# Kernel tuning notes

Measured on AMD Instinct MI355X. Metric: run time of the kernel, lower is better.

The kernel has to match this reference:

```python
import jax, jax.numpy as jnp
import numpy as np

D_MODEL = 1024
N_HEADS = 16
HEAD_DIM = D_MODEL // N_HEADS
D_FF = 4096
RANK = 8
B, T = 4, 2048


def _layernorm(x, g, b, eps=1e-5):
    mu = jnp.mean(x, axis=-1, keepdims=True)
    var = jnp.var(x, axis=-1, keepdims=True)
    return (x - mu) * jax.lax.rsqrt(var + eps) * g + b


def _dyn_linear(x, W, A, b_dyn, bias=None):
    # base: x [b,t,i] @ W.T  (W is [o,i] like nn.Linear)
    out = jnp.einsum('bti,oi->bto', x, W)
    if bias is not None:
        out = out + bias
    # per-sample low-rank delta: (x @ b_dyn.T) @ A.T
    delta = jnp.einsum('bti,bri,or->bto', x, b_dyn, A)
    return out + delta


def setup_inputs() -> dict:
    key = jax.random.key(0)
    ks = jax.random.split(key, 24)
    s = 0.02
    inp = {
        'x': jax.random.normal(ks[0], (B, T, D_MODEL), jnp.float32),
        'dyn_q': jax.random.normal(ks[1], (B, RANK, D_MODEL), jnp.float32) * s,
        'dyn_k': jax.random.normal(ks[2], (B, RANK, D_MODEL), jnp.float32) * s,
        'dyn_v': jax.random.normal(ks[3], (B, RANK, D_MODEL), jnp.float32) * s,
        'dyn_ff1': jax.random.normal(ks[4], (B, RANK, D_MODEL), jnp.float32) * s,
        'dyn_ff2': jax.random.normal(ks[5], (B, RANK, D_FF), jnp.float32) * s,
        'Wq': jax.random.normal(ks[6], (D_MODEL, D_MODEL), jnp.float32) / np.sqrt(D_MODEL),
        'Aq': jax.random.normal(ks[7], (D_MODEL, RANK), jnp.float32) * s,
        'Wk': jax.random.normal(ks[8], (D_MODEL, D_MODEL), jnp.float32) / np.sqrt(D_MODEL),
        'Ak': jax.random.normal(ks[9], (D_MODEL, RANK), jnp.float32) * s,
        'Wv': jax.random.normal(ks[10], (D_MODEL, D_MODEL), jnp.float32) / np.sqrt(D_MODEL),
        'Av': jax.random.normal(ks[11], (D_MODEL, RANK), jnp.float32) * s,
        'Wo': jax.random.normal(ks[12], (D_MODEL, D_MODEL), jnp.float32) / np.sqrt(D_MODEL),
        'W1': jax.random.normal(ks[13], (D_FF, D_MODEL), jnp.float32) / np.sqrt(D_MODEL),
        'b1': jnp.zeros((D_FF,), jnp.float32),
        'A1': jax.random.normal(ks[14], (D_FF, RANK), jnp.float32) * s,
        'W2': jax.random.normal(ks[15], (D_MODEL, D_FF), jnp.float32) / np.sqrt(D_FF),
        'b2': jnp.zeros((D_MODEL,), jnp.float32),
        'A2': jax.random.normal(ks[16], (D_MODEL, RANK), jnp.float32) * s,
        'g1': jnp.ones((D_MODEL,), jnp.float32),
        'beta1': jnp.zeros((D_MODEL,), jnp.float32),
        'g2': jnp.ones((D_MODEL,), jnp.float32),
        'beta2': jnp.zeros((D_MODEL,), jnp.float32),
    }
    return inp


def reference(x, dyn_q, dyn_k, dyn_v, dyn_ff1, dyn_ff2,
              Wq, Aq, Wk, Ak, Wv, Av, Wo,
              W1, b1, A1, W2, b2, A2,
              g1, beta1, g2, beta2):
    bsz, seq_len, _ = x.shape
    residual = x
    h = _layernorm(x, g1, beta1)
    q = _dyn_linear(h, Wq, Aq, dyn_q)
    k = _dyn_linear(h, Wk, Ak, dyn_k)
    v = _dyn_linear(h, Wv, Av, dyn_v)
    # [b, t, h, d] -> [b, h, t, d]
    q = q.reshape(bsz, seq_len, N_HEADS, HEAD_DIM).transpose(0, 2, 1, 3)
    k = k.reshape(bsz, seq_len, N_HEADS, HEAD_DIM).transpose(0, 2, 1, 3)
    v = v.reshape(bsz, seq_len, N_HEADS, HEAD_DIM).transpose(0, 2, 1, 3)
    score = jnp.einsum('bhqd,bhkd->bhqk', q, k) / np.sqrt(HEAD_DIM).astype(np.float32)
    attn = jax.nn.softmax(score, axis=-1)
    ctx = jnp.einsum('bhqk,bhkd->bhqd', attn, v)
    ctx = ctx.transpose(0, 2, 1, 3).reshape(bsz, seq_len, D_MODEL)
    x = residual + jnp.einsum('bti,oi->bto', ctx, Wo)  # dropout p=0
    residual = x
    h = _layernorm(x, g2, beta2)
    ff = jax.nn.gelu(_dyn_linear(h, W1, A1, dyn_ff1, bias=b1), approximate=False)
    ff = _dyn_linear(ff, W2, A2, dyn_ff2, bias=b2)
    return residual + ff
```

## Files before the change

### kernel.cpp

```cpp
#include <hip/hip_runtime.h>
#include <math.h>

#define D_MODEL 1024
#define D_FF    4096
#define RANK    8
#define BATCH   4
#define SEQ     2048
#define MTOT    (BATCH*SEQ)
#define NHEADS  16
#define HDIM    64

typedef __attribute__((ext_vector_type(8))) __bf16 bf16x8;
typedef __attribute__((ext_vector_type(4))) float f32x4;
typedef __attribute__((ext_vector_type(8))) unsigned short u16x8;
typedef __attribute__((ext_vector_type(4))) unsigned short u16x4;

__device__ __forceinline__ unsigned short f2bf(float f) {
  __bf16 h = (__bf16)f;
  return __builtin_bit_cast(unsigned short, h);
}
__device__ __forceinline__ float bf2f(unsigned short h) {
  union { unsigned int u; float f; } v; v.u = ((unsigned int)h) << 16;
  return v.f;
}

__device__ __forceinline__ f32x4 mfma16(bf16x8 a, bf16x8 b, f32x4 c) {
  return __builtin_amdgcn_mfma_f32_16x16x32_bf16(a, b, c, 0, 0, 0);
}

#define GLDS(g, l) __builtin_amdgcn_global_load_lds( \
    (const __attribute__((address_space(1))) void*)(g), \
    (__attribute__((address_space(3))) void*)(l), 16, 0, 0)

__global__ __launch_bounds__(256) void cvt_bf16(const float* __restrict__ in,
                                                unsigned short* __restrict__ out, int n8)
{
  int i = blockIdx.x * 256 + threadIdx.x;
  if (i >= n8) return;
  const float4 a  = *reinterpret_cast<const float4*>(in + (size_t)i * 8);
  const float4 b  = *reinterpret_cast<const float4*>(in + (size_t)i * 8 + 4);
  u16x8 o;
  o[0] = f2bf(a.x); o[1] = f2bf(a.y); o[2] = f2bf(a.z); o[3] = f2bf(a.w);
  o[4] = f2bf(b.x); o[5] = f2bf(b.y); o[6] = f2bf(b.z); o[7] = f2bf(b.w);
  *reinterpret_cast<u16x8*>(out + (size_t)i * 8) = o;
}

__global__ __launch_bounds__(256) void ln_fwd(const float* __restrict__ x,
                                              const float* __restrict__ g,
                                              const float* __restrict__ be,
                                              unsigned short* __restrict__ out)
{
  const int row = blockIdx.x;
  const int t = threadIdx.x;
  const float* xr = x + (size_t)row * D_MODEL;
  float4 vv = *reinterpret_cast<const float4*>(xr + t * 4);
  float s  = vv.x + vv.y + vv.z + vv.w;
  float s2 = vv.x * vv.x + vv.y * vv.y + vv.z * vv.z + vv.w * vv.w;
#pragma unroll
  for (int mm = 1; mm < 64; mm <<= 1) { s += __shfl_xor(s, mm); s2 += __shfl_xor(s2, mm); }
  __shared__ float red[8];
  const int w = t >> 6, l = t & 63;
  if (l == 0) { red[w] = s; red[4 + w] = s2; }
  __syncthreads();
  s  = red[0] + red[1] + red[2] + red[3];
  s2 = red[4] + red[5] + red[6] + red[7];
  float mean = s * (1.f / D_MODEL);
  float var  = s2 * (1.f / D_MODEL) - mean * mean;
  float rstd = rsqrtf(var + 1e-5f);
  float4 gv = *reinterpret_cast<const float4*>(g  + t * 4);
  float4 bv = *reinterpret_cast<const float4*>(be + t * 4);
  u16x4 o;
  o[0] = f2bf((vv.x - mean) * rstd * gv.x + bv.x);
  o[1] = f2bf((vv.y - mean) * rstd * gv.y + bv.y);
  o[2] = f2bf((vv.z - mean) * rstd * gv.z + bv.z);
  o[3] = f2bf((vv.w - mean) * rstd * gv.w + bv.w);
  *reinterpret_cast<u16x4*>(out + (size_t)row * D_MODEL + t * 4) = o;
}

template<int ILEN>
__global__ __launch_bounds__(256) void dyn_u(const unsigned short* __restrict__ hmat,
                                             const float* __restrict__ dyn,
                                             float* __restrict__ u)
{
  const int tid = threadIdx.x, w = tid >> 6, l = tid & 63;
  const int m0 = blockIdx.x * 16 + w * 4;
  const int b = m0 / SEQ;
  const float* dynb = dyn + (size_t)b * RANK * ILEN;
  float acc[4][RANK] = {};
  for (int s = 0; s < ILEN / 64; ++s) {
    const int i = l + s * 64;
    float hv[4];
#pragma unroll
    for (int rr = 0; rr < 4; ++rr) hv[rr] = bf2f(hmat[(size_t)(m0 + rr) * ILEN + i]);
#pragma unroll
    for (int r = 0; r < RANK; ++r) {
      float d = dynb[(size_t)r * ILEN + i];
#pragma unroll
      for (int rr = 0; rr < 4; ++rr) acc[rr][r] += hv[rr] * d;
    }
  }
#pragma unroll
  for (int rr = 0; rr < 4; ++rr)
#pragma unroll
    for (int r = 0; r < RANK; ++r) {
      float a = acc[rr][r];
#pragma unroll
      for (int mm = 1; mm < 64; mm <<= 1) a += __shfl_xor(a, mm);
      if (l == 0) u[(size_t)(m0 + rr) * RANK + r] = a;
    }
}

__global__ __launch_bounds__(256) void dyn_u_qkv(const unsigned short* __restrict__ hmat,
                                                 const float* __restrict__ dq,
                                                 const float* __restrict__ dk,
                                                 const float* __restrict__ dv,
                                                 float* __restrict__ u)
{
  const int tid = threadIdx.x, w = tid >> 6, l = tid & 63;
  const int m0 = blockIdx.x * 16 + w * 4;
  const int b = m0 / SEQ;
  const float* db0 = dq + (size_t)b * RANK * D_MODEL;
  const float* db1 = dk + (size_t)b * RANK * D_MODEL;
  const float* db2 = dv + (size_t)b * RANK * D_MODEL;
  float acc[4][3 * RANK] = {};
  for (int s = 0; s < D_MODEL / 64; ++s) {
    const int i = l + s * 64;
    float hv[4];
#pragma unroll
    for (int rr = 0; rr < 4; ++rr) hv[rr] = bf2f(hmat[(size_t)(m0 + rr) * D_MODEL + i]);
#pragma unroll
    for (int r = 0; r < RANK; ++r) {
      float d0 = db0[(size_t)r * D_MODEL + i];
      float d1 = db1[(size_t)r * D_MODEL + i];
      float d2 = db2[(size_t)r * D_MODEL + i];
#pragma unroll
      for (int rr = 0; rr < 4; ++rr) {
        acc[rr][r] += hv[rr] * d0;
        acc[rr][RANK + r] += hv[rr] * d1;
        acc[rr][2 * RANK + r] += hv[rr] * d2;
      }
    }
  }
#pragma unroll
  for (int g = 0; g < 3; ++g)
#pragma unroll
    for (int rr = 0; rr < 4; ++rr)
#pragma unroll
      for (int r = 0; r < RANK; ++r) {
        float a = acc[rr][g * RANK + r];
#pragma unroll
        for (int mm = 1; mm < 64; mm <<= 1) a += __shfl_xor(a, mm);
        if (l == 0) u[((size_t)g * MTOT + m0 + rr) * RANK + r] = a;
      }
}

template<int NDIM, int KDIM, int MODE>
__global__ __launch_bounds__(512, 2) void gemm_bt(const unsigned short* __restrict__ A,
                                                  const unsigned short* __restrict__ B,
                                                  void* __restrict__ outp,
                                                  void* __restrict__ outp2,
                                                  const float* __restrict__ uvec,
                                                  const float* __restrict__ Ad0,
                                                  const float* __restrict__ Ad1,
                                                  const float* __restrict__ Ad2,
                                                  const float* __restrict__ bias,
                                                  const float* __restrict__ resid)
{
  constexpr bool HAS_DYN = (MODE == 2 || MODE == 3 || MODE == 5);
  __shared__ unsigned short sAB[2][(256 + 128) * 64];
  const int tid = threadIdx.x;
  const int w = tid >> 6, l = tid & 63;

  constexpr int NBX = NDIM / 128;
  constexpr int NWG = NBX * (MTOT / 256);
  const int bid = blockIdx.y * NBX + blockIdx.x;
  const int sbid = (bid & 7) * (NWG / 8) + (bid >> 3);
  const int tm = (sbid / NBX) * 256, tn = (sbid % NBX) * 128;
  const int wm = w >> 1, wn = w & 1;

  f32x4 acc[4][4] = {};

  const int srow = l >> 3;
  const int sc8 = (l & 7) ^ (srow & 7);
  const unsigned short* Ag = A + (size_t)(tm + srow) * KDIM + sc8 * 8;
  const unsigned short* Bg = B + (size_t)(tn + srow) * KDIM + sc8 * 8;

  const int arow = wm * 64 + (l & 15);
  const int bcol = wn * 64 + (l & 15);
  const int kb0 = l >> 4;
  const int swz = l & 7;

  constexpr int NT = KDIM / 64;

  auto stage = [&](int buf, int kt) {
    unsigned short* bA = &sAB[buf][0];
    unsigned short* bB = &sAB[buf][256 * 64];
#pragma unroll
    for (int it = 0; it < 4; ++it) {
      const int st = w * 4 + it;
      GLDS(Ag + (size_t)(st * 8) * KDIM + kt, bA + st * 512);
    }
#pragma unroll
    for (int it = 0; it < 2; ++it) {
      const int st = w * 2 + it;
      GLDS(Bg + (size_t)(st * 8) * KDIM + kt, bB + st * 512);
    }
  };

  stage(0, 0);
  asm volatile("s_waitcnt vmcnt(0)" ::: "memory");
  __syncthreads();

  int cur = 0;
  for (int t = 0; t < NT; ++t) {
    if (t + 1 < NT) stage(cur ^ 1, (t + 1) * 64);

    const unsigned short* sA_ = &sAB[cur][0];
    const unsigned short* sB_ = &sAB[cur][256 * 64];
#pragma unroll
    for (int kk = 0; kk < 2; ++kk) {
      bf16x8 af[4], bfv[4];
      const int kphys = ((kk * 4 + kb0) ^ swz) << 3;
#pragma unroll
      for (int i = 0; i < 4; ++i)
        af[i] = *reinterpret_cast<const bf16x8*>(&sA_[(arow + i * 16) * 64 + kphys]);
#pragma unroll
      for (int j = 0; j < 4; ++j)
        bfv[j] = *reinterpret_cast<const bf16x8*>(&sB_[(bcol + j * 16) * 64 + kphys]);
#pragma unroll
      for (int i = 0; i < 4; ++i)
#pragma unroll
        for (int j = 0; j < 4; ++j)
          acc[i][j] = mfma16(af[i], bfv[j], acc[i][j]);
    }
    __syncthreads();
    cur ^= 1;
  }

  const int rbase = tm + wm * 64 + ((l >> 4) << 2);
  const int cbase = tn + wn * 64 + (l & 15);

  const int seg = tn >> 10;
  const float* Ad = Ad0;
  const float* uv = uvec;
  if constexpr (MODE == 5) {
    Ad = (seg == 0) ? Ad0 : (seg == 1) ? Ad1 : Ad2;
    uv = uvec + (size_t)seg * ((size_t)MTOT * RANK);
  }

#pragma unroll
  for (int i = 0; i < 4; ++i) {
    float uu[4][8];
    if constexpr (HAS_DYN) {
#pragma unroll
      for (int r = 0; r < 4; ++r) {
        const float* up = uv + (size_t)(rbase + i * 16 + r) * RANK;
#pragma unroll
        for (int p = 0; p < 8; ++p) uu[r][p] = up[p];
      }
    }
#pragma unroll
    for (int j = 0; j < 4; ++j) {
      const int col = cbase + j * 16;
      float ad[8];
      if constexpr (HAS_DYN) {
#pragma unroll
        for (int p = 0; p < 8; ++p) ad[p] = Ad[(size_t)col * RANK + p];
      }
      float vv4[4];
#pragma unroll
      for (int r = 0; r < 4; ++r) {
        const int row = rbase + i * 16 + r;
        float v = acc[i][j][r];
        if constexpr (HAS_DYN) {
#pragma unroll
          for (int p = 0; p < 8; ++p) v += uu[r][p] * ad[p];
        }
        if constexpr (MODE == 2) {
          v += bias[col];
          v = 0.5f * v * (1.f + erff(v * 0.70710678118654752f));
        }
        if constexpr (MODE == 1) {
          v += resid[(size_t)row * NDIM + col];
        }
        if constexpr (MODE == 3) {
          v += bias[col] + resid[(size_t)row * NDIM + col];
        }
        if constexpr (MODE == 5) {
          if (seg == 0) v *= 0.18033688011112042f;
        }
        vv4[r] = v;
      }
      if constexpr (MODE == 2) {
#pragma unroll
        for (int r = 0; r < 4; ++r)
          ((unsigned short*)outp)[(size_t)(rbase + i * 16 + r) * NDIM + col] = f2bf(vv4[r]);
      } else if constexpr (MODE == 5) {
        const int cl = col & 1023;
        if (seg < 2) {
#pragma unroll
          for (int r = 0; r < 4; ++r)
            ((unsigned short*)outp)[((size_t)seg * MTOT + rbase + i * 16 + r) * D_MODEL + cl] =
                f2bf(vv4[r]);
        } else {
          const int row0 = rbase + i * 16;
          const int bb = row0 >> 11, t0 = row0 & (SEQ - 1);
          const int hh = cl >> 6, dd = cl & 63;
          const int jj = (t0 >> 4) & 3;
          unsigned short* vb = &((unsigned short*)outp2)[
              (((size_t)bb * NHEADS + hh) * HDIM + dd) * SEQ + (t0 & ~63)];
#pragma unroll
          for (int dlt = 0; dlt < 4; ++dlt)
            vb[((t0 & 15) + dlt) * 4 + jj] = f2bf(vv4[dlt]);
        }
      } else {
#pragma unroll
        for (int r = 0; r < 4; ++r)
          ((float*)outp)[(size_t)(rbase + i * 16 + r) * NDIM + col] = vv4[r];
      }
    }
  }
}

__global__ __launch_bounds__(256, 4) void attn_fwd(const unsigned short* __restrict__ q,
                                                   const unsigned short* __restrict__ k,
                                                   const unsigned short* __restrict__ vt,
                                                   unsigned short* __restrict__ ctx)
{
  __shared__ unsigned short sK[128 * 64];
  __shared__ unsigned short sV[64 * 128];
  __shared__ unsigned short sP[4][32 * 64];

  const int tid = threadIdx.x, w = tid >> 6, l = tid & 63;
  const int lin = blockIdx.y * (SEQ / 128) + blockIdx.x;
  const int W = (lin & 7) * ((BATCH * NHEADS * SEQ / 128) / 8) + (lin >> 3);
  const int bh = W >> 4, b = bh >> 4, hh = bh & 15;
  const int q0 = (W & 15) * 128 + w * 32;
  const size_t base = ((size_t)b * SEQ) * D_MODEL + hh * HDIM;
  const size_t vtbase = (size_t)bh * HDIM * SEQ;

  bf16x8 qf[2][2];
#pragma unroll
  for (int i = 0; i < 2; ++i)
#pragma unroll
    for (int ks = 0; ks < 2; ++ks)
      qf[i][ks] = *reinterpret_cast<const bf16x8*>(
          &q[base + (size_t)(q0 + i * 16 + (l & 15)) * D_MODEL + ks * 32 + (l >> 4) * 8]);

  float mrun[2][4], lrun[2][4];
  f32x4 oacc[2][4] = {};
#pragma unroll
  for (int i = 0; i < 2; ++i)
#pragma unroll
    for (int r = 0; r < 4; ++r) { mrun[i][r] = -3.0e38f; lrun[i][r] = 0.f; }

  const int krow_l = l >> 3;
  const int kswz = (l & 7) ^ (krow_l & 7);
  const unsigned short* kg = k + base + (size_t)krow_l * D_MODEL + kswz * 8;
  const int vrow_l = l >> 4;
  const int vswz = (l & 15) ^ (((w & 1) * 4 + vrow_l) & 7);
  const unsigned short* vg = vt + vtbase + (size_t)vrow_l * SEQ + vswz * 8;

  const int swz = l & 7;
  const int kb0 = l >> 4;

  for (int kt = 0; kt < SEQ; kt += 128) {
    __syncthreads();
#pragma unroll
    for (int it = 0; it < 4; ++it) {
      const int r4 = it * 4 + w;
      GLDS(kg + (size_t)(kt + r4 * 8) * D_MODEL, sK + r4 * 512);
      GLDS(vg + (size_t)(r4 * 4) * SEQ + kt, sV + r4 * 512);
    }
    asm volatile("s_waitcnt vmcnt(0)" ::: "memory");
    __syncthreads();

    f32x4 sacc[2][8] = {};
    __builtin_amdgcn_s_setprio(1);
#pragma unroll
    for (int ks = 0; ks < 2; ++ks) {
#pragma unroll
      for (int j = 0; j < 8; ++j) {
        const int row = j * 16 + (l & 15);
        bf16x8 kf = *reinterpret_cast<const bf16x8*>(
            &sK[row * 64 + (((ks * 4 + kb0) ^ swz) << 3)]);
#pragma unroll
        for (int i = 0; i < 2; ++i) sacc[i][j] = mfma16(qf[i][ks], kf, sacc[i][j]);
      }
    }
    __builtin_amdgcn_s_setprio(0);

    float pr[2][4][4];
    const int c15 = l & 15;
#pragma unroll
    for (int i = 0; i < 2; ++i) {
#pragma unroll
      for (int r = 0; r < 4; ++r) {
        float sv[8];
#pragma unroll
        for (int j = 0; j < 8; ++j) sv[j] = sacc[i][j][r];
        float mx = fmaxf(fmaxf(fmaxf(sv[0], sv[1]), fmaxf(sv[2], sv[3])),
                         fmaxf(fmaxf(sv[4], sv[5]), fmaxf(sv[6], sv[7])));
#pragma unroll
        for (int mm = 1; mm < 16; mm <<= 1) mx = fmaxf(mx, __shfl_xor(mx, mm, 16));
        const float mnew = fmaxf(mrun[i][r], mx);
        const float alpha = __builtin_exp2f(mrun[i][r] - mnew);
        mrun[i][r] = mnew;
        float p[8], ps = 0.f;
#pragma unroll
        for (int j = 0; j < 8; ++j) { p[j] = __builtin_exp2f(sv[j] - mnew); ps += p[j]; }
#pragma unroll
        for (int mm = 1; mm < 16; mm <<= 1) ps += __shfl_xor(ps, mm, 16);
        lrun[i][r] = lrun[i][r] * alpha + ps;
        const int prow = i * 16 + ((l >> 4) << 2) + r;
        u16x4 pk;
        pk[0] = f2bf(p[0]); pk[1] = f2bf(p[1]); pk[2] = f2bf(p[2]); pk[3] = f2bf(p[3]);
        *reinterpret_cast<u16x4*>(
            &sP[w][prow * 64 + ((((c15 >> 1) ^ (prow & 7)) << 3) | ((c15 & 1) << 2))]) = pk;
#pragma unroll
        for (int jj = 0; jj < 4; ++jj) pr[i][r][jj] = p[4 + jj];
#pragma unroll
        for (int j = 0; j < 4; ++j) oacc[i][j][r] *= alpha;
      }
    }

    __builtin_amdgcn_s_setprio(1);
#pragma unroll
    for (int ks = 0; ks < 2; ++ks) {
      bf16x8 pf[2];
#pragma unroll
      for (int i = 0; i < 2; ++i) {
        const int prw = i * 16 + (l & 15);
        pf[i] = *reinterpret_cast<const bf16x8*>(
            &sP[w][prw * 64 + (((ks * 4 + kb0) ^ (prw & 7)) << 3)]);
      }
#pragma unroll
      for (int j = 0; j < 4; ++j) {
        const int row = j * 16 + (l & 15);
        bf16x8 vf = *reinterpret_cast<const bf16x8*>(
            &sV[row * 128 + (((ks * 4 + kb0) ^ swz) << 3)]);
#pragma unroll
        for (int i = 0; i < 2; ++i) oacc[i][j] = mfma16(pf[i], vf, oacc[i][j]);
      }
    }
    __builtin_amdgcn_s_setprio(0);

#pragma unroll
    for (int i = 0; i < 2; ++i) {
#pragma unroll
      for (int r = 0; r < 4; ++r) {
        const int prow = i * 16 + ((l >> 4) << 2) + r;
        u16x4 pk;
        pk[0] = f2bf(pr[i][r][0]); pk[1] = f2bf(pr[i][r][1]);
        pk[2] = f2bf(pr[i][r][2]); pk[3] = f2bf(pr[i][r][3]);
        *reinterpret_cast<u16x4*>(
            &sP[w][prow * 64 + ((((c15 >> 1) ^ (prow & 7)) << 3) | ((c15 & 1) << 2))]) = pk;
      }
    }

    __builtin_amdgcn_s_setprio(1);
#pragma unroll
    for (int ks = 0; ks < 2; ++ks) {
      bf16x8 pf[2];
#pragma unroll
      for (int i = 0; i < 2; ++i) {
        const int prw = i * 16 + (l & 15);
        pf[i] = *reinterpret_cast<const bf16x8*>(
            &sP[w][prw * 64 + (((ks * 4 + kb0) ^ (prw & 7)) << 3)]);
      }
#pragma unroll
      for (int j = 0; j < 4; ++j) {
        const int row = j * 16 + (l & 15);
        bf16x8 vf = *reinterpret_cast<const bf16x8*>(
            &sV[row * 128 + (((8 + ks * 4 + kb0) ^ swz) << 3)]);
#pragma unroll
        for (int i = 0; i < 2; ++i) oacc[i][j] = mfma16(pf[i], vf, oacc[i][j]);
      }
    }
    __builtin_amdgcn_s_setprio(0);
  }

#pragma unroll
  for (int i = 0; i < 2; ++i)
#pragma unroll
    for (int r = 0; r < 4; ++r) {
      float inv = 1.f / lrun[i][r];
      int row = q0 + i * 16 + ((l >> 4) << 2) + r;
#pragma unroll
      for (int j = 0; j < 4; ++j)
        ctx[base + (size_t)row * D_MODEL + j * 16 + (l & 15)] = f2bf(oacc[i][j][r] * inv);
    }
}

extern "C" void kernel_launch(void* const* d_in, const int* in_sizes, int n_in,
                              void* d_out, int out_size, void* d_ws, size_t ws_size,
                              hipStream_t stream)
{
  (void)in_sizes; (void)n_in; (void)out_size; (void)ws_size;
  const float* x      = (const float*)d_in[0];
  const float* dyn_q  = (const float*)d_in[1];
  const float* dyn_k  = (const float*)d_in[2];
  const float* dyn_v  = (const float*)d_in[3];
  const float* dyn_f1 = (const float*)d_in[4];
  const float* dyn_f2 = (const float*)d_in[5];
  const float* Wq = (const float*)d_in[6];
  const float* Aq = (const float*)d_in[7];
  const float* Wk = (const float*)d_in[8];
  const float* Ak = (const float*)d_in[9];
  const float* Wv = (const float*)d_in[10];
  const float* Av = (const float*)d_in[11];
  const float* Wo = (const float*)d_in[12];
  const float* W1 = (const float*)d_in[13];
  const float* b1 = (const float*)d_in[14];
  const float* A1 = (const float*)d_in[15];
  const float* W2 = (const float*)d_in[16];
  const float* b2 = (const float*)d_in[17];
  const float* A2 = (const float*)d_in[18];
  const float* g1 = (const float*)d_in[19];
  const float* be1 = (const float*)d_in[20];
  const float* g2 = (const float*)d_in[21];
  const float* be2 = (const float*)d_in[22];

  char* ws = (char*)d_ws;
  size_t o = 0;
  auto take = [&](size_t b) { size_t r = o; o += (b + 255) & ~(size_t)255; return r; };
  const size_t o_wq = take((size_t)D_MODEL * D_MODEL * 2);
  const size_t o_wk = take((size_t)D_MODEL * D_MODEL * 2);
  const size_t o_wv = take((size_t)D_MODEL * D_MODEL * 2);
  const size_t o_wo = take((size_t)D_MODEL * D_MODEL * 2);
  const size_t o_w1 = take((size_t)D_FF * D_MODEL * 2);
  const size_t o_w2 = take((size_t)D_FF * D_MODEL * 2);
  const size_t o_h1 = take((size_t)MTOT * D_MODEL * 2);
  const size_t o_q  = take((size_t)MTOT * D_MODEL * 2);
  const size_t o_k  = take((size_t)MTOT * D_MODEL * 2);
  const size_t o_v  = take((size_t)MTOT * D_MODEL * 2);
  const size_t o_u  = take((size_t)MTOT * RANK * 4 * 3);
  const size_t o_ff = take((size_t)MTOT * D_FF * 2);

  unsigned short* wq_b = (unsigned short*)(ws + o_wq);
  unsigned short* wk_b = (unsigned short*)(ws + o_wk);
  unsigned short* wv_b = (unsigned short*)(ws + o_wv);
  unsigned short* wo_b = (unsigned short*)(ws + o_wo);
  unsigned short* w1_b = (unsigned short*)(ws + o_w1);
  unsigned short* w2_b = (unsigned short*)(ws + o_w2);
  unsigned short* h1   = (unsigned short*)(ws + o_h1);
  unsigned short* qb   = (unsigned short*)(ws + o_q);
  unsigned short* vtb  = (unsigned short*)(ws + o_v);
  float* u_q  = (float*)(ws + o_u);
  float* u_k  = u_q + (size_t)MTOT * RANK;
  unsigned short* ctx = h1;
  float* x2 = (float*)(ws + o_q);
  unsigned short* h2 = vtb;
  float* u_f1 = u_q;
  float* u_f2 = u_k;
  unsigned short* ffb = (unsigned short*)(ws + o_ff);

  cvt_bf16<<<512,  256, 0, stream>>>(Wq, wq_b, (D_MODEL * D_MODEL) / 8);
  cvt_bf16<<<512,  256, 0, stream>>>(Wk, wk_b, (D_MODEL * D_MODEL) / 8);
  cvt_bf16<<<512,  256, 0, stream>>>(Wv, wv_b, (D_MODEL * D_MODEL) / 8);
  cvt_bf16<<<512,  256, 0, stream>>>(Wo, wo_b, (D_MODEL * D_MODEL) / 8);
  cvt_bf16<<<2048, 256, 0, stream>>>(W1, w1_b, (D_FF * D_MODEL) / 8);
  cvt_bf16<<<2048, 256, 0, stream>>>(W2, w2_b, (D_FF * D_MODEL) / 8);

  ln_fwd<<<MTOT, 256, 0, stream>>>(x, g1, be1, h1);

  dyn_u_qkv<<<MTOT / 16, 256, 0, stream>>>(h1, dyn_q, dyn_k, dyn_v, u_q);

  gemm_bt<3 * D_MODEL, D_MODEL, 5><<<dim3(3 * D_MODEL / 128, MTOT / 256), 512, 0, stream>>>(
      h1, wq_b, qb, vtb, u_q, Aq, Ak, Av, nullptr, nullptr);

  attn_fwd<<<dim3(SEQ / 128, BATCH * NHEADS), 256, 0, stream>>>(
      qb, qb + (size_t)MTOT * D_MODEL, vtb, ctx);

  gemm_bt<D_MODEL, D_MODEL, 1><<<dim3(D_MODEL / 128, MTOT / 256), 512, 0, stream>>>(
      ctx, wo_b, x2, nullptr, nullptr, nullptr, nullptr, nullptr, nullptr, x);

  ln_fwd<<<MTOT, 256, 0, stream>>>(x2, g2, be2, h2);

  dyn_u<D_MODEL><<<MTOT / 16, 256, 0, stream>>>(h2, dyn_f1, u_f1);
  gemm_bt<D_FF, D_MODEL, 2><<<dim3(D_FF / 128, MTOT / 256), 512, 0, stream>>>(
      h2, w1_b, ffb, nullptr, u_f1, A1, nullptr, nullptr, b1, nullptr);

  dyn_u<D_FF><<<MTOT / 16, 256, 0, stream>>>(ffb, dyn_f2, u_f2);
  gemm_bt<D_MODEL, D_FF, 3><<<dim3(D_MODEL / 128, MTOT / 256), 512, 0, stream>>>(
      ffb, w2_b, (float*)d_out, nullptr, u_f2, A2, nullptr, nullptr, b2, x2);
}
```

Measured before the change: 621.3 us.

## Widen GEMM N-tile to 256, lazy softmax rescale, fuse weight conversions

The GEMM becomes templated on the N tile width, and the QKV and FF1 GEMMs now use 256x256 tiles with one workgroup per CU. The aim is better operand reuse, paid for with more LDS and registers and lower occupancy. Attention switches to a lazy online-softmax rescale that only updates the running max when it grows by more than a threshold, which skips most exp and multiply work on the accumulators. The six weight conversion launches are merged into one kernel to cut launch overhead.

```diff
diff --git a/kernel.cpp b/kernel.cpp
--- a/kernel.cpp
+++ b/kernel.cpp
@@ -32,17 +32,29 @@
     (const __attribute__((address_space(1))) void*)(g), \
     (__attribute__((address_space(3))) void*)(l), 16, 0, 0)
 
-__global__ __launch_bounds__(256) void cvt_bf16(const float* __restrict__ in,
-                                                unsigned short* __restrict__ out, int n8)
+__global__ __launch_bounds__(256) void cvt_bf16_all(
+    const float* __restrict__ s0, const float* __restrict__ s1,
+    const float* __restrict__ s2, const float* __restrict__ s3,
+    const float* __restrict__ s4, const float* __restrict__ s5,
+    unsigned short* __restrict__ d0, unsigned short* __restrict__ d1,
+    unsigned short* __restrict__ d2, unsigned short* __restrict__ d3,
+    unsigned short* __restrict__ d4, unsigned short* __restrict__ d5)
 {
-  int i = blockIdx.x * 256 + threadIdx.x;
-  if (i >= n8) return;
-  const float4 a  = *reinterpret_cast<const float4*>(in + (size_t)i * 8);
-  const float4 b  = *reinterpret_cast<const float4*>(in + (size_t)i * 8 + 4);
+  const int b = blockIdx.x;
+  const float* src; unsigned short* dst; int base;
+  if (b < 512)       { src = s0; dst = d0; base = b; }
+  else if (b < 1024) { src = s1; dst = d1; base = b - 512; }
+  else if (b < 1536) { src = s2; dst = d2; base = b - 1024; }
+  else if (b < 2048) { src = s3; dst = d3; base = b - 1536; }
+  else if (b < 4096) { src = s4; dst = d4; base = b - 2048; }
+  else               { src = s5; dst = d5; base = b - 4096; }
+  const size_t i = (size_t)base * 256 + threadIdx.x;
+  const float4 a  = *reinterpret_cast<const float4*>(src + i * 8);
+  const float4 c  = *reinterpret_cast<const float4*>(src + i * 8 + 4);
   u16x8 o;
   o[0] = f2bf(a.x); o[1] = f2bf(a.y); o[2] = f2bf(a.z); o[3] = f2bf(a.w);
-  o[4] = f2bf(b.x); o[5] = f2bf(b.y); o[6] = f2bf(b.z); o[7] = f2bf(b.w);
-  *reinterpret_cast<u16x8*>(out + (size_t)i * 8) = o;
+  o[4] = f2bf(c.x); o[5] = f2bf(c.y); o[6] = f2bf(c.z); o[7] = f2bf(c.w);
+  *reinterpret_cast<u16x8*>(dst + i * 8) = o;
 }
 
 __global__ __launch_bounds__(256) void ln_fwd(const float* __restrict__ x,
@@ -154,38 +166,43 @@
       }
 }
 
-template<int NDIM, int KDIM, int MODE>
-__global__ __launch_bounds__(512, 2) void gemm_bt(const unsigned short* __restrict__ A,
-                                                  const unsigned short* __restrict__ B,
-                                                  void* __restrict__ outp,
-                                                  void* __restrict__ outp2,
-                                                  const float* __restrict__ uvec,
-                                                  const float* __restrict__ Ad0,
-                                                  const float* __restrict__ Ad1,
-                                                  const float* __restrict__ Ad2,
-                                                  const float* __restrict__ bias,
-                                                  const float* __restrict__ resid)
+template<int NDIM, int KDIM, int MODE, int BN>
+__global__ __launch_bounds__(512, (BN == 256) ? 1 : 2)
+void gemm_bt(const unsigned short* __restrict__ A,
+             const unsigned short* __restrict__ B,
+             void* __restrict__ outp,
+             void* __restrict__ outp2,
+             const float* __restrict__ uvec,
+             const float* __restrict__ Ad0,
+             const float* __restrict__ Ad1,
+             const float* __restrict__ Ad2,
+             const float* __restrict__ bias,
+             const float* __restrict__ resid)
 {
   constexpr bool HAS_DYN = (MODE == 2 || MODE == 3 || MODE == 5);
-  __shared__ unsigned short sAB[2][(256 + 128) * 64];
+  constexpr int WN = BN / 64;
+  constexpr int WM = 8 / WN;
+  constexpr int MSPAN = 256 / WM;
+  constexpr int NI = MSPAN / 16;
+  __shared__ unsigned short sAB[2][(256 + BN) * 64];
   const int tid = threadIdx.x;
   const int w = tid >> 6, l = tid & 63;
 
-  constexpr int NBX = NDIM / 128;
+  constexpr int NBX = NDIM / BN;
   constexpr int NWG = NBX * (MTOT / 256);
   const int bid = blockIdx.y * NBX + blockIdx.x;
   const int sbid = (bid & 7) * (NWG / 8) + (bid >> 3);
-  const int tm = (sbid / NBX) * 256, tn = (sbid % NBX) * 128;
-  const int wm = w >> 1, wn = w & 1;
-
-  f32x4 acc[4][4] = {};
+  const int tm = (sbid / NBX) * 256, tn = (sbid % NBX) * BN;
+  const int wm = w / WN, wn = w % WN;
+
+  f32x4 acc[NI][4] = {};
 
   const int srow = l >> 3;
   const int sc8 = (l & 7) ^ (srow & 7);
   const unsigned short* Ag = A + (size_t)(tm + srow) * KDIM + sc8 * 8;
   const unsigned short* Bg = B + (size_t)(tn + srow) * KDIM + sc8 * 8;
 
-  const int arow = wm * 64 + (l & 15);
+  const int arow = wm * MSPAN + (l & 15);
   const int bcol = wn * 64 + (l & 15);
   const int kb0 = l >> 4;
   const int swz = l & 7;
@@ -201,8 +218,8 @@
       GLDS(Ag + (size_t)(st * 8) * KDIM + kt, bA + st * 512);
     }
 #pragma unroll
-    for (int it = 0; it < 2; ++it) {
-      const int st = w * 2 + it;
+    for (int it = 0; it < WN; ++it) {
+      const int st = w * WN + it;
       GLDS(Bg + (size_t)(st * 8) * KDIM + kt, bB + st * 512);
     }
   };
@@ -219,16 +236,16 @@
     const unsigned short* sB_ = &sAB[cur][256 * 64];
 #pragma unroll
     for (int kk = 0; kk < 2; ++kk) {
-      bf16x8 af[4], bfv[4];
+      bf16x8 af[NI], bfv[4];
       const int kphys = ((kk * 4 + kb0) ^ swz) << 3;
 #pragma unroll
-      for (int i = 0; i < 4; ++i)
+      for (int i = 0; i < NI; ++i)
         af[i] = *reinterpret_cast<const bf16x8*>(&sA_[(arow + i * 16) * 64 + kphys]);
 #pragma unroll
       for (int j = 0; j < 4; ++j)
         bfv[j] = *reinterpret_cast<const bf16x8*>(&sB_[(bcol + j * 16) * 64 + kphys]);
 #pragma unroll
-      for (int i = 0; i < 4; ++i)
+      for (int i = 0; i < NI; ++i)
 #pragma unroll
         for (int j = 0; j < 4; ++j)
           acc[i][j] = mfma16(af[i], bfv[j], acc[i][j]);
@@ -237,7 +254,7 @@
     cur ^= 1;
   }
 
-  const int rbase = tm + wm * 64 + ((l >> 4) << 2);
+  const int rbase = tm + wm * MSPAN + ((l >> 4) << 2);
   const int cbase = tn + wn * 64 + (l & 15);
 
   const int seg = tn >> 10;
@@ -249,7 +266,7 @@
   }
 
 #pragma unroll
-  for (int i = 0; i < 4; ++i) {
+  for (int i = 0; i < NI; ++i) {
     float uu[4][8];
     if constexpr (HAS_DYN) {
 #pragma unroll
@@ -403,15 +420,20 @@
                          fmaxf(fmaxf(sv[4], sv[5]), fmaxf(sv[6], sv[7])));
 #pragma unroll
         for (int mm = 1; mm < 16; mm <<= 1) mx = fmaxf(mx, __shfl_xor(mx, mm, 16));
-        const float mnew = fmaxf(mrun[i][r], mx);
-        const float alpha = __builtin_exp2f(mrun[i][r] - mnew);
-        mrun[i][r] = mnew;
+        if (mx > mrun[i][r] + 12.f) {
+          const float alpha = __builtin_exp2f(mrun[i][r] - mx);
+          mrun[i][r] = mx;
+          lrun[i][r] *= alpha;
+#pragma unroll
+          for (int j = 0; j < 4; ++j) oacc[i][j][r] *= alpha;
+        }
+        const float m = mrun[i][r];
         float p[8], ps = 0.f;
 #pragma unroll
-        for (int j = 0; j < 8; ++j) { p[j] = __builtin_exp2f(sv[j] - mnew); ps += p[j]; }
+        for (int j = 0; j < 8; ++j) { p[j] = __builtin_exp2f(sv[j] - m); ps += p[j]; }
 #pragma unroll
         for (int mm = 1; mm < 16; mm <<= 1) ps += __shfl_xor(ps, mm, 16);
-        lrun[i][r] = lrun[i][r] * alpha + ps;
+        lrun[i][r] += ps;
         const int prow = i * 16 + ((l >> 4) << 2) + r;
         u16x4 pk;
         pk[0] = f2bf(p[0]); pk[1] = f2bf(p[1]); pk[2] = f2bf(p[2]); pk[3] = f2bf(p[3]);
@@ -419,8 +441,6 @@
             &sP[w][prow * 64 + ((((c15 >> 1) ^ (prow & 7)) << 3) | ((c15 & 1) << 2))]) = pk;
 #pragma unroll
         for (int jj = 0; jj < 4; ++jj) pr[i][r][jj] = p[4 + jj];
-#pragma unroll
-        for (int j = 0; j < 4; ++j) oacc[i][j][r] *= alpha;
       }
     }
 
@@ -555,33 +575,29 @@
   float* u_f2 = u_k;
   unsigned short* ffb = (unsigned short*)(ws + o_ff);
 
-  cvt_bf16<<<512,  256, 0, stream>>>(Wq, wq_b, (D_MODEL * D_MODEL) / 8);
-  cvt_bf16<<<512,  256, 0, stream>>>(Wk, wk_b, (D_MODEL * D_MODEL) / 8);
-  cvt_bf16<<<512,  256, 0, stream>>>(Wv, wv_b, (D_MODEL * D_MODEL) / 8);
-  cvt_bf16<<<512,  256, 0, stream>>>(Wo, wo_b, (D_MODEL * D_MODEL) / 8);
-  cvt_bf16<<<2048, 256, 0, stream>>>(W1, w1_b, (D_FF * D_MODEL) / 8);
-  cvt_bf16<<<2048, 256, 0, stream>>>(W2, w2_b, (D_FF * D_MODEL) / 8);
+  cvt_bf16_all<<<6144, 256, 0, stream>>>(Wq, Wk, Wv, Wo, W1, W2,
+                                         wq_b, wk_b, wv_b, wo_b, w1_b, w2_b);
 
   ln_fwd<<<MTOT, 256, 0, stream>>>(x, g1, be1, h1);
 
   dyn_u_qkv<<<MTOT / 16, 256, 0, stream>>>(h1, dyn_q, dyn_k, dyn_v, u_q);
 
-  gemm_bt<3 * D_MODEL, D_MODEL, 5><<<dim3(3 * D_MODEL / 128, MTOT / 256), 512, 0, stream>>>(
+  gemm_bt<3 * D_MODEL, D_MODEL, 5, 256><<<dim3(3 * D_MODEL / 256, MTOT / 256), 512, 0, stream>>>(
       h1, wq_b, qb, vtb, u_q, Aq, Ak, Av, nullptr, nullptr);
 
   attn_fwd<<<dim3(SEQ / 128, BATCH * NHEADS), 256, 0, stream>>>(
       qb, qb + (size_t)MTOT * D_MODEL, vtb, ctx);
 
-  gemm_bt<D_MODEL, D_MODEL, 1><<<dim3(D_MODEL / 128, MTOT / 256), 512, 0, stream>>>(
+  gemm_bt<D_MODEL, D_MODEL, 1, 128><<<dim3(D_MODEL / 128, MTOT / 256), 512, 0, stream>>>(
       ctx, wo_b, x2, nullptr, nullptr, nullptr, nullptr, nullptr, nullptr, x);
 
   ln_fwd<<<MTOT, 256, 0, stream>>>(x2, g2, be2, h2);
 
   dyn_u<D_MODEL><<<MTOT / 16, 256, 0, stream>>>(h2, dyn_f1, u_f1);
-  gemm_bt<D_FF, D_MODEL, 2><<<dim3(D_FF / 128, MTOT / 256), 512, 0, stream>>>(
+  gemm_bt<D_FF, D_MODEL, 2, 256><<<dim3(D_FF / 256, MTOT / 256), 512, 0, stream>>>(
       h2, w1_b, ffb, nullptr, u_f1, A1, nullptr, nullptr, b1, nullptr);
 
   dyn_u<D_FF><<<MTOT / 16, 256, 0, stream>>>(ffb, dyn_f2, u_f2);
-  gemm_bt<D_MODEL, D_FF, 3><<<dim3(D_MODEL / 128, MTOT / 256), 512, 0, stream>>>(
+  gemm_bt<D_MODEL, D_FF, 3, 128><<<dim3(D_MODEL / 128, MTOT / 256), 512, 0, stream>>>(
       ffb, w2_b, (float*)d_out, nullptr, u_f2, A2, nullptr, nullptr, b2, x2);
 }
```

Result: slower. 728.0 us (+17.2%).
